# Optimization experiments

Measured on AMD Instinct MI355X. Metric: run time of the kernel, lower is better.

## Reference

```python
import jax, jax.numpy as jnp
import numpy as np

B = 8388608  # batch

def setup_inputs() -> dict:
    key = jax.random.key(0)
    ks = jax.random.split(key, 7)
    x = jax.random.normal(ks[0], (B, 2), dtype=jnp.float32)
    # PyTorch Linear: y = x @ W.T + b, W shape [out, in]
    W1 = jax.random.normal(ks[1], (3, 2), dtype=jnp.float32) * 0.5
    b1 = jax.random.normal(ks[2], (3,), dtype=jnp.float32) * 0.1
    W2 = jax.random.normal(ks[3], (2, 3), dtype=jnp.float32) * 0.5
    b2 = jax.random.normal(ks[4], (2,), dtype=jnp.float32) * 0.1
    W3 = jax.random.normal(ks[5], (1, 2), dtype=jnp.float32) * 0.5
    b3 = jax.random.normal(ks[6], (1,), dtype=jnp.float32) * 0.1
    return {"x": x, "W1": W1, "b1": b1, "W2": W2, "b2": b2, "W3": W3, "b3": b3}

def reference(x, W1, b1, W2, b2, W3, b3):
    h1 = jax.nn.relu(x @ W1.T + b1)          # [B, 3]
    h2 = jax.nn.relu(h1 @ W2.T + b2)         # [B, 2]
    out = jax.nn.sigmoid((h2 @ W3.T + b3).squeeze(-1))  # [B]
    return (out, h1, h2)
```

## Files before the change

### kernel.cpp

```cpp
#include <hip/hip_runtime.h>
#include <math.h>


__global__ __launch_bounds__(256) void mlp321_kernel(
    const float* __restrict__ x,
    const float* __restrict__ W1, const float* __restrict__ b1,
    const float* __restrict__ W2, const float* __restrict__ b2,
    const float* __restrict__ W3, const float* __restrict__ b3,
    float* __restrict__ out_p, float* __restrict__ h1_p, float* __restrict__ h2_p,
    int nrows)
{
    const int t = blockIdx.x * blockDim.x + threadIdx.x;
    const int row0 = t * 4;
    if (row0 >= nrows) return;

    float w1[6], w2[6], w3v[2], bb1[3], bb2[2], bb3;
#pragma unroll
    for (int i = 0; i < 6; ++i) w1[i] = W1[i];
#pragma unroll
    for (int i = 0; i < 3; ++i) bb1[i] = b1[i];
#pragma unroll
    for (int i = 0; i < 6; ++i) w2[i] = W2[i];
#pragma unroll
    for (int i = 0; i < 2; ++i) bb2[i] = b2[i];
    w3v[0] = W3[0]; w3v[1] = W3[1];
    bb3 = b3[0];

    const float4* xv = reinterpret_cast<const float4*>(x + (size_t)row0 * 2);
    float4 xa = xv[0];
    float4 xb = xv[1];
    float xr[4][2] = {{xa.x, xa.y}, {xa.z, xa.w}, {xb.x, xb.y}, {xb.z, xb.w}};

    float h1v[4][3], h2v[4][2], ov[4];
#pragma unroll
    for (int r = 0; r < 4; ++r) {
        const float x0 = xr[r][0], x1 = xr[r][1];
#pragma unroll
        for (int j = 0; j < 3; ++j) {
            float v = fmaf(x0, w1[j * 2 + 0], fmaf(x1, w1[j * 2 + 1], bb1[j]));
            h1v[r][j] = v > 0.f ? v : 0.f;
        }
#pragma unroll
        for (int k = 0; k < 2; ++k) {
            float v = bb2[k];
#pragma unroll
            for (int j = 0; j < 3; ++j) v = fmaf(h1v[r][j], w2[k * 3 + j], v);
            h2v[r][k] = v > 0.f ? v : 0.f;
        }
        float z = fmaf(h2v[r][0], w3v[0], fmaf(h2v[r][1], w3v[1], bb3));
        ov[r] = 1.f / (1.f + __expf(-z));
    }

    reinterpret_cast<float4*>(out_p + row0)[0] = make_float4(ov[0], ov[1], ov[2], ov[3]);

    float4* h1v4 = reinterpret_cast<float4*>(h1_p + (size_t)row0 * 3);
    h1v4[0] = make_float4(h1v[0][0], h1v[0][1], h1v[0][2], h1v[1][0]);
    h1v4[1] = make_float4(h1v[1][1], h1v[1][2], h1v[2][0], h1v[2][1]);
    h1v4[2] = make_float4(h1v[2][2], h1v[3][0], h1v[3][1], h1v[3][2]);

    float4* h2v4 = reinterpret_cast<float4*>(h2_p + (size_t)row0 * 2);
    h2v4[0] = make_float4(h2v[0][0], h2v[0][1], h2v[1][0], h2v[1][1]);
    h2v4[1] = make_float4(h2v[2][0], h2v[2][1], h2v[3][0], h2v[3][1]);
}

extern "C" void kernel_launch(void* const* d_in, const int* in_sizes, int n_in,
                              void* d_out, int out_size, void* d_ws, size_t ws_size,
                              hipStream_t stream) {
    const float* x  = (const float*)d_in[0];
    const float* W1 = (const float*)d_in[1];
    const float* b1 = (const float*)d_in[2];
    const float* W2 = (const float*)d_in[3];
    const float* b2 = (const float*)d_in[4];
    const float* W3 = (const float*)d_in[5];
    const float* b3 = (const float*)d_in[6];

    const int B = in_sizes[0] / 2;
    float* out_p = (float*)d_out;
    float* h1_p  = out_p + (size_t)B;
    float* h2_p  = h1_p + (size_t)B * 3;

    const int threads = 256;
    const int rows_per_thread = 4;
    const int blocks = (B + threads * rows_per_thread - 1) / (threads * rows_per_thread);
    mlp321_kernel<<<blocks, threads, 0, stream>>>(x, W1, b1, W2, b2, W3, b3,
                                                  out_p, h1_p, h2_p, B);
}
```

Baseline: 265.5 us.

## Stage outputs in shared memory for fully coalesced nontemporal stores

Each block now processes 1024 rows, writing h1, h2 and the sigmoid output into shared memory first. After a barrier, threads write the staged tile back with contiguous, warp-coalesced float4 nontemporal stores. Input loads are also rearranged so adjacent threads read adjacent float4s. This targets the strided per-thread vector stores of the previous layout, at the cost of an LDS round trip, a block barrier and some LDS bank conflicts on the stride-3 writes.

```diff
diff --git a/kernel.cpp b/kernel.cpp
--- a/kernel.cpp
+++ b/kernel.cpp
@@ -1,6 +1,10 @@
 #include <hip/hip_runtime.h>
 #include <math.h>
 
+
+#define RPB 1024
+
+typedef float v4f __attribute__((ext_vector_type(4)));
 
 __global__ __launch_bounds__(256) void mlp321_kernel(
     const float* __restrict__ x,
@@ -10,9 +14,12 @@
     float* __restrict__ out_p, float* __restrict__ h1_p, float* __restrict__ h2_p,
     int nrows)
 {
-    const int t = blockIdx.x * blockDim.x + threadIdx.x;
-    const int row0 = t * 4;
-    if (row0 >= nrows) return;
+    __shared__ __align__(16) float s_h1[RPB * 3];
+    __shared__ __align__(16) float s_h2[RPB * 2];
+    __shared__ __align__(16) float s_out[RPB];
+
+    const int tid = threadIdx.x;
+    const size_t base = (size_t)blockIdx.x * RPB;
 
     float w1[6], w2[6], w3v[2], bb1[3], bb2[2], bb3;
 #pragma unroll
@@ -26,41 +33,73 @@
     w3v[0] = W3[0]; w3v[1] = W3[1];
     bb3 = b3[0];
 
-    const float4* xv = reinterpret_cast<const float4*>(x + (size_t)row0 * 2);
-    float4 xa = xv[0];
-    float4 xb = xv[1];
-    float xr[4][2] = {{xa.x, xa.y}, {xa.z, xa.w}, {xb.x, xb.y}, {xb.z, xb.w}};
+    const bool full = (base + RPB) <= (size_t)nrows;
 
-    float h1v[4][3], h2v[4][2], ov[4];
+    const v4f* xv = reinterpret_cast<const v4f*>(x + base * 2);
 #pragma unroll
-    for (int r = 0; r < 4; ++r) {
-        const float x0 = xr[r][0], x1 = xr[r][1];
+    for (int it = 0; it < 2; ++it) {
+        const int idx = it * 256 + tid;
+        const int r0 = idx * 2;
+        if (!full && (base + r0) >= (size_t)nrows) continue;
+        v4f xa = xv[idx];
+        float xr[2][2] = {{xa.x, xa.y}, {xa.z, xa.w}};
 #pragma unroll
-        for (int j = 0; j < 3; ++j) {
-            float v = fmaf(x0, w1[j * 2 + 0], fmaf(x1, w1[j * 2 + 1], bb1[j]));
-            h1v[r][j] = v > 0.f ? v : 0.f;
+        for (int r = 0; r < 2; ++r) {
+            const int row = r0 + r;
+            if (!full && (base + row) >= (size_t)nrows) continue;
+            const float x0 = xr[r][0], x1 = xr[r][1];
+            float h1v[3];
+#pragma unroll
+            for (int j = 0; j < 3; ++j) {
+                float v = fmaf(x0, w1[j * 2 + 0], fmaf(x1, w1[j * 2 + 1], bb1[j]));
+                h1v[j] = v > 0.f ? v : 0.f;
+                s_h1[row * 3 + j] = h1v[j];
+            }
+            float h2v[2];
+#pragma unroll
+            for (int k = 0; k < 2; ++k) {
+                float v = bb2[k];
+#pragma unroll
+                for (int j = 0; j < 3; ++j) v = fmaf(h1v[j], w2[k * 3 + j], v);
+                h2v[k] = v > 0.f ? v : 0.f;
+                s_h2[row * 2 + k] = h2v[k];
+            }
+            float z = fmaf(h2v[0], w3v[0], fmaf(h2v[1], w3v[1], bb3));
+            s_out[row] = 1.f / (1.f + __expf(-z));
+        }
+    }
+    __syncthreads();
+
+    if (full) {
+        const v4f* so = reinterpret_cast<const v4f*>(s_out);
+        const v4f* s1 = reinterpret_cast<const v4f*>(s_h1);
+        const v4f* s2 = reinterpret_cast<const v4f*>(s_h2);
+        v4f* po = reinterpret_cast<v4f*>(out_p + base);
+        v4f* p1 = reinterpret_cast<v4f*>(h1_p + base * 3);
+        v4f* p2 = reinterpret_cast<v4f*>(h2_p + base * 2);
+
+        __builtin_nontemporal_store(so[tid], po + tid);
+#pragma unroll
+        for (int it = 0; it < 3; ++it) {
+            const int i = it * 256 + tid;
+            __builtin_nontemporal_store(s1[i], p1 + i);
         }
 #pragma unroll
-        for (int k = 0; k < 2; ++k) {
-            float v = bb2[k];
-#pragma unroll
-            for (int j = 0; j < 3; ++j) v = fmaf(h1v[r][j], w2[k * 3 + j], v);
-            h2v[r][k] = v > 0.f ? v : 0.f;
+        for (int it = 0; it < 2; ++it) {
+            const int i = it * 256 + tid;
+            __builtin_nontemporal_store(s2[i], p2 + i);
         }
-        float z = fmaf(h2v[r][0], w3v[0], fmaf(h2v[r][1], w3v[1], bb3));
-        ov[r] = 1.f / (1.f + __expf(-z));
+    } else {
+        const int remain = (int)((size_t)nrows - base);
+        for (int r = tid; r < remain; r += 256) {
+            out_p[base + r] = s_out[r];
+            h1_p[(base + r) * 3 + 0] = s_h1[r * 3 + 0];
+            h1_p[(base + r) * 3 + 1] = s_h1[r * 3 + 1];
+            h1_p[(base + r) * 3 + 2] = s_h1[r * 3 + 2];
+            h2_p[(base + r) * 2 + 0] = s_h2[r * 2 + 0];
+            h2_p[(base + r) * 2 + 1] = s_h2[r * 2 + 1];
+        }
     }
-
-    reinterpret_cast<float4*>(out_p + row0)[0] = make_float4(ov[0], ov[1], ov[2], ov[3]);
-
-    float4* h1v4 = reinterpret_cast<float4*>(h1_p + (size_t)row0 * 3);
-    h1v4[0] = make_float4(h1v[0][0], h1v[0][1], h1v[0][2], h1v[1][0]);
-    h1v4[1] = make_float4(h1v[1][1], h1v[1][2], h1v[2][0], h1v[2][1]);
-    h1v4[2] = make_float4(h1v[2][2], h1v[3][0], h1v[3][1], h1v[3][2]);
-
-    float4* h2v4 = reinterpret_cast<float4*>(h2_p + (size_t)row0 * 2);
-    h2v4[0] = make_float4(h2v[0][0], h2v[0][1], h2v[1][0], h2v[1][1]);
-    h2v4[1] = make_float4(h2v[2][0], h2v[2][1], h2v[3][0], h2v[3][1]);
 }
 
 extern "C" void kernel_launch(void* const* d_in, const int* in_sizes, int n_in,
@@ -79,9 +118,7 @@
     float* h1_p  = out_p + (size_t)B;
     float* h2_p  = h1_p + (size_t)B * 3;
 
-    const int threads = 256;
-    const int rows_per_thread = 4;
-    const int blocks = (B + threads * rows_per_thread - 1) / (threads * rows_per_thread);
-    mlp321_kernel<<<blocks, threads, 0, stream>>>(x, W1, b1, W2, b2, W3, b3,
-                                                  out_p, h1_p, h2_p, B);
+    const int blocks = (B + RPB - 1) / RPB;
+    mlp321_kernel<<<blocks, 256, 0, stream>>>(x, W1, b1, W2, b2, W3, b3,
+                                              out_p, h1_p, h2_p, B);
 }
```

Result: faster. 257.1 us (-3.2%).
